# Kernel tuning notes

Hardware: AMD Instinct MI355X
Metric: run time of the kernel (lower is better)

Reference implementation:

```python
import jax, jax.numpy as jnp
import numpy as np

NUM_HEADS = 12
EPS = 1e-6


def setup_inputs() -> dict:
    key = jax.random.key(0)
    k1, k2, k3, k4 = jax.random.split(key, 4)
    N, B, D = 1025, 8, 768
    x = jax.random.normal(k1, (N, B, D), dtype=jnp.float32)
    # torch nn.Linear weights: [out_features, in_features]
    w_qkv = jax.random.normal(k2, (3 * D, D), dtype=jnp.float32) * (D ** -0.5)
    w_proj = jax.random.normal(k3, (D, D), dtype=jnp.float32) * (D ** -0.5)
    b_proj = jax.random.normal(k4, (D,), dtype=jnp.float32) * 0.01
    return {"x": x, "w_qkv": w_qkv, "w_proj": w_proj, "b_proj": b_proj}


def reference(x, w_qkv, w_proj, b_proj):
    N, B, D = x.shape
    H = NUM_HEADS
    hd = D // H
    scale = hd ** -0.5
    scale_vv = scale * 1.0  # scale_multiplier = 1.0

    xb = jnp.transpose(x, (1, 0, 2))  # [B, N, D]
    qkv = xb @ w_qkv.T  # [B, N, 3D]
    qkv = qkv.reshape(B, N, 3, H, hd).transpose(2, 0, 3, 1, 4)  # [3, B, H, N, hd]
    q, k, v = qkv[0], qkv[1], qkv[2]

    # QK path: only row 0 of out_ori survives the masking, compute just that row
    scores0 = jnp.einsum('bhqd,bhkd->bhqk', q[:, :, :1], k) * scale  # [B,H,1,N]
    attn0 = jax.nn.softmax(scores0, axis=-1)
    out0 = jnp.einsum('bhqk,bhkd->bhqd', attn0, v)  # [B,H,1,hd]

    # VV cosine path: only rows 1: survive
    vn = v / jnp.maximum(jnp.linalg.norm(v, axis=-1, keepdims=True), EPS)
    scores_vv = jnp.einsum('bhqd,bhkd->bhqk', vn[:, :, 1:], vn) * scale_vv  # [B,H,N-1,N]
    attn_vv = jax.nn.softmax(scores_vv, axis=-1)
    out_vv = jnp.einsum('bhqk,bhkd->bhqd', attn_vv, v)  # [B,H,N-1,hd]

    out = jnp.concatenate([out0, out_vv], axis=2)  # [B,H,N,hd]
    out = out.transpose(0, 2, 1, 3).reshape(B, N, D)
    out = out @ w_proj.T + b_proj
    return jnp.transpose(out, (1, 0, 2))  # [N, B, D]
```

## Files before the change

### kernel.cpp

```cpp
#include <hip/hip_runtime.h>

typedef unsigned short u16;
typedef unsigned int   u32;
typedef __attribute__((ext_vector_type(8))) short short8;
typedef __attribute__((ext_vector_type(4))) float f32x4;

#define AS1 __attribute__((address_space(1)))
#define AS3 __attribute__((address_space(3)))

#define NSEQ  1025
#define BB    8
#define DD    768
#define HH    12
#define MROWS 8200
#define MPAD  8320
#define KPAD  1088

__device__ __forceinline__ void gl2lds16(const void* g, void* l) {
  __builtin_amdgcn_global_load_lds((const AS1 u32*)g, (AS3 u32*)l, 16, 0, 0);
}
__device__ __forceinline__ u16 f2bf(float f) {
  u32 u = __float_as_uint(f);
  return (u16)((u + 0x7FFFu + ((u >> 16) & 1u)) >> 16);
}
__device__ __forceinline__ float bf2f(u16 u) { return __uint_as_float(((u32)u) << 16); }

__global__ __launch_bounds__(256) void prep(const float* __restrict__ x,
                                            const float* __restrict__ wqkv,
                                            const float* __restrict__ wproj,
                                            u16* __restrict__ xb,
                                            u16* __restrict__ wkv,
                                            u16* __restrict__ wpj) {
  const int XB_G  = MPAD * 192;
  const int WKV_G = 1536 * 192;
  const int WPJ_G = 768 * 192;
  int g = blockIdx.x * 256 + threadIdx.x;
  float4 v;
  u16* dst;
  size_t di;
  if (g < XB_G) {
    int m = g / 192, e4 = g - m * 192;
    if (m < MROWS) {
      int bb = m / NSEQ, ns = m - bb * NSEQ;
      v = ((const float4*)x)[(size_t)(ns * BB + bb) * 192 + e4];
    } else {
      v.x = v.y = v.z = v.w = 0.f;
    }
    dst = xb; di = (size_t)g;
  } else if (g < XB_G + WKV_G) {
    int r = g - XB_G;
    v = ((const float4*)wqkv)[(size_t)147456 + r];
    dst = wkv; di = (size_t)r;
  } else if (g < XB_G + WKV_G + WPJ_G) {
    int r = g - XB_G - WKV_G;
    v = ((const float4*)wproj)[r];
    dst = wpj; di = (size_t)r;
  } else {
    return;
  }
  uint2 o;
  o.x = (u32)f2bf(v.x) | ((u32)f2bf(v.y) << 16);
  o.y = (u32)f2bf(v.z) | ((u32)f2bf(v.w) << 16);
  ((uint2*)dst)[di] = o;
}

template <int MODE, int NT>
__global__ __launch_bounds__(256) void gemm_bt(const u16* __restrict__ A,
                                               const u16* __restrict__ W,
                                               u16* __restrict__ Cbf,
                                               float* __restrict__ Cf,
                                               const float* __restrict__ bias,
                                               int ldc) {
  __shared__ u16 sA[128 * 64];
  __shared__ u16 sW[128 * 64];
  const int id = blockIdx.x;
  const int rx = id & 7, qx = id >> 3;
  const int kq = qx / NT;
  const int m_t = rx + (kq << 3);
  if (m_t > 64) return;
  const int n_t = qx - kq * NT;
  const int m0 = m_t << 7, n0 = n_t << 7;

  const int tid = threadIdx.x;
  const int w = tid >> 6, lane = tid & 63;
  const int wm = w & 1, wn = w >> 1;
  const int lc = lane & 15, lr = lane >> 4;

  f32x4 zero4 = {0.f, 0.f, 0.f, 0.f};
  f32x4 acc[4][4];
#pragma unroll
  for (int i = 0; i < 4; ++i)
#pragma unroll
    for (int j = 0; j < 4; ++j) acc[i][j] = zero4;

  const int r0 = tid >> 3;
  const int ko = (tid & 7) << 3;
  const u16* gA = A + (size_t)(m0 + r0) * DD + ko;
  const u16* gW = W + (size_t)(n0 + r0) * DD + ko;
  char* lA = (char*)sA + tid * 16;
  char* lW = (char*)sW + tid * 16;

#pragma unroll 1
  for (int kt = 0; kt < 12; ++kt) {
    __syncthreads();
#pragma unroll
    for (int j = 0; j < 4; ++j) {
      gl2lds16(gA + (size_t)j * 32 * DD + kt * 64, lA + j * 4096);
      gl2lds16(gW + (size_t)j * 32 * DD + kt * 64, lW + j * 4096);
    }
    __syncthreads();
#pragma unroll
    for (int kk = 0; kk < 2; ++kk) {
      short8 af[4], wf[4];
#pragma unroll
      for (int mt = 0; mt < 4; ++mt)
        af[mt] = *(const short8*)((char*)sA + ((wm << 6) + (mt << 4) + lc) * 128 + (kk << 6) + (lr << 4));
#pragma unroll
      for (int nt = 0; nt < 4; ++nt)
        wf[nt] = *(const short8*)((char*)sW + ((wn << 6) + (nt << 4) + lc) * 128 + (kk << 6) + (lr << 4));
#pragma unroll
      for (int mt = 0; mt < 4; ++mt)
#pragma unroll
        for (int nt = 0; nt < 4; ++nt)
          acc[mt][nt] = __builtin_amdgcn_mfma_f32_16x16x32_bf16(af[mt], wf[nt], acc[mt][nt], 0, 0, 0);
    }
  }

  if (MODE == 0) {
#pragma unroll
    for (int mt = 0; mt < 4; ++mt)
#pragma unroll
      for (int r = 0; r < 4; ++r) {
        int m = m0 + (wm << 6) + (mt << 4) + (lr << 2) + r;
        if (m < MROWS) {
          size_t base = (size_t)m * ldc + n0 + (wn << 6) + lc;
#pragma unroll
          for (int nt = 0; nt < 4; ++nt) Cbf[base + (nt << 4)] = f2bf(acc[mt][nt][r]);
        }
      }
  } else {
    float b4[4];
#pragma unroll
    for (int nt = 0; nt < 4; ++nt) b4[nt] = bias[n0 + (wn << 6) + (nt << 4) + lc];
#pragma unroll
    for (int mt = 0; mt < 4; ++mt)
#pragma unroll
      for (int r = 0; r < 4; ++r) {
        int m = m0 + (wm << 6) + (mt << 4) + (lr << 2) + r;
        if (m < MROWS) {
          int bb = m / NSEQ;
          int ns = m - bb * NSEQ;
          float* o = Cf + (size_t)ns * (BB * DD) + bb * DD + n0 + (wn << 6) + lc;
#pragma unroll
          for (int nt = 0; nt < 4; ++nt) o[nt << 4] = acc[mt][nt][r] + b4[nt];
        }
      }
  }
}

__global__ __launch_bounds__(256) void q0_kernel(const float* __restrict__ x,
                                                 const float* __restrict__ wq,
                                                 float* __restrict__ q0) {
  __shared__ float red[256];
  int bid = blockIdx.x;
  int b = bid / HH, c = bid - b * HH;
  int tid = threadIdx.x;
  int dp = (c << 6) + (tid >> 2), part = tid & 3;
  const float4* x4 = (const float4*)(x + (size_t)b * DD + part * 192);
  const float4* w4 = (const float4*)(wq + (size_t)dp * DD + part * 192);
  float acc = 0.f;
#pragma unroll 4
  for (int e = 0; e < 48; ++e) {
    float4 a = x4[e], w = w4[e];
    acc += a.x * w.x + a.y * w.y + a.z * w.z + a.w * w.w;
  }
  red[tid] = acc;
  __syncthreads();
  if (part == 0) q0[b * DD + dp] = red[tid] + red[tid + 1] + red[tid + 2] + red[tid + 3];
}

__global__ __launch_bounds__(256) void transpose_v(const u16* __restrict__ kv,
                                                   u16* __restrict__ vT,
                                                   u16* __restrict__ vn) {
  __shared__ u16 tile[64][72];
  __shared__ float red[256];
  __shared__ float sInv[64];
  int bid = blockIdx.x;
  int kc = bid % 17;
  int t2 = bid / 17;
  int h = t2 % HH, b = t2 / HH;
  int tid = threadIdx.x;
  int kl = tid >> 2, dc = (tid & 3) << 4;
  int key = kc * 64 + kl;
  u32 vals[8];
  if (key < NSEQ) {
    const u32* g = (const u32*)(kv + ((size_t)b * NSEQ + key) * 1536 + DD + h * 64 + dc);
#pragma unroll
    for (int i = 0; i < 8; ++i) vals[i] = g[i];
  } else {
#pragma unroll
    for (int i = 0; i < 8; ++i) vals[i] = 0;
  }
  float part = 0.f;
#pragma unroll
  for (int i = 0; i < 8; ++i) {
    float a = bf2f((u16)(vals[i] & 0xFFFF));
    float c = bf2f((u16)(vals[i] >> 16));
    part += a * a + c * c;
    ((u32*)&tile[kl][dc])[i] = vals[i];
  }
  red[tid] = part;
  __syncthreads();
  if ((tid & 3) == 0) {
    float s = red[tid] + red[tid + 1] + red[tid + 2] + red[tid + 3];
    sInv[kl] = (key < NSEQ) ? 1.0f / fmaxf(sqrtf(s), 1e-6f) : 0.0f;
  }
  __syncthreads();
  float iv = sInv[kl];
  u32 ovn[8];
#pragma unroll
  for (int i = 0; i < 8; ++i) {
    float a = bf2f((u16)(vals[i] & 0xFFFF)) * iv;
    float c = bf2f((u16)(vals[i] >> 16)) * iv;
    ovn[i] = (u32)f2bf(a) | ((u32)f2bf(c) << 16);
  }
  u32* on = (u32*)(vn + ((size_t)(b * HH + h) * KPAD + key) * 64 + dc);
#pragma unroll
  for (int i = 0; i < 8; ++i) on[i] = ovn[i];
  int dl = tid >> 2, ks = (tid & 3) << 4;
  u32 ov[8];
#pragma unroll
  for (int i = 0; i < 8; ++i)
    ov[i] = (u32)tile[ks + 2 * i][dl] | ((u32)tile[ks + 2 * i + 1][dl] << 16);
  u16* o = vT + (size_t)(b * HH + h) * 64 * KPAD + (size_t)dl * KPAD + kc * 64 + ks;
#pragma unroll
  for (int i = 0; i < 8; ++i) ((u32*)o)[i] = ov[i];
}

__global__ __launch_bounds__(256) void row0_attn(const float* __restrict__ q0,
                                                 const u16* __restrict__ kv,
                                                 u16* __restrict__ attn) {
  __shared__ float sq[64];
  __shared__ float sc[NSEQ];
  __shared__ float red[256];
  __shared__ float rpv[32][68];
  int bid = blockIdx.x;
  int b = bid / HH, h = bid - b * HH;
  int tid = threadIdx.x;
  if (tid < 64) sq[tid] = q0[b * DD + h * 64 + tid];
  __syncthreads();
  float mx = -1e30f;
  for (int n = tid; n < NSEQ; n += 256) {
    const u32* kr = (const u32*)(kv + ((size_t)b * NSEQ + n) * 1536 + h * 64);
    float s = 0.f;
#pragma unroll
    for (int i = 0; i < 32; ++i) {
      u32 u = kr[i];
      s += bf2f((u16)(u & 0xFFFF)) * sq[2 * i] + bf2f((u16)(u >> 16)) * sq[2 * i + 1];
    }
    s *= 0.125f;
    sc[n] = s;
    mx = fmaxf(mx, s);
  }
  red[tid] = mx;
  __syncthreads();
  for (int st = 128; st > 0; st >>= 1) {
    if (tid < st) red[tid] = fmaxf(red[tid], red[tid + st]);
    __syncthreads();
  }
  mx = red[0];
  __syncthreads();
  float ds = 0.f;
  for (int n = tid; n < NSEQ; n += 256) {
    float p = __expf(sc[n] - mx);
    sc[n] = p;
    ds += p;
  }
  red[tid] = ds;
  __syncthreads();
  for (int st = 128; st > 0; st >>= 1) {
    if (tid < st) red[tid] += red[tid + st];
    __syncthreads();
  }
  float den = red[0];
  __syncthreads();

  int kp = tid >> 3, dc = (tid & 7) << 3;
  const u16* vb = kv + (size_t)b * NSEQ * 1536 + DD + h * 64 + dc;
  float acc[8];
#pragma unroll
  for (int i = 0; i < 8; ++i) acc[i] = 0.f;
#pragma unroll 4
  for (int j = 0; j < 32; ++j) {
    int n = kp + (j << 5);
    uint4 v = *(const uint4*)(vb + (size_t)n * 1536);
    float p = sc[n];
    acc[0] += p * bf2f((u16)(v.x & 0xFFFF));
    acc[1] += p * bf2f((u16)(v.x >> 16));
    acc[2] += p * bf2f((u16)(v.y & 0xFFFF));
    acc[3] += p * bf2f((u16)(v.y >> 16));
    acc[4] += p * bf2f((u16)(v.z & 0xFFFF));
    acc[5] += p * bf2f((u16)(v.z >> 16));
    acc[6] += p * bf2f((u16)(v.w & 0xFFFF));
    acc[7] += p * bf2f((u16)(v.w >> 16));
  }
  if (kp == 0) {
    uint4 v = *(const uint4*)(vb + (size_t)1024 * 1536);
    float p = sc[1024];
    acc[0] += p * bf2f((u16)(v.x & 0xFFFF));
    acc[1] += p * bf2f((u16)(v.x >> 16));
    acc[2] += p * bf2f((u16)(v.y & 0xFFFF));
    acc[3] += p * bf2f((u16)(v.y >> 16));
    acc[4] += p * bf2f((u16)(v.z & 0xFFFF));
    acc[5] += p * bf2f((u16)(v.z >> 16));
    acc[6] += p * bf2f((u16)(v.w & 0xFFFF));
    acc[7] += p * bf2f((u16)(v.w >> 16));
  }
#pragma unroll
  for (int i = 0; i < 8; ++i) rpv[kp][dc + i] = acc[i];
  __syncthreads();
  if (tid < 64) {
    float s = 0.f;
#pragma unroll
    for (int p = 0; p < 32; ++p) s += rpv[p][tid];
    attn[(size_t)b * NSEQ * DD + h * 64 + tid] = f2bf(s / den);
  }
}

__global__ __launch_bounds__(256) void vv_attn(const u16* __restrict__ vn,
                                               const u16* __restrict__ vT,
                                               u16* __restrict__ attn) {
  __shared__ u16 sQ[2 * 128 * 32];
  __shared__ u16 sK[2 * 64 * 32];
  __shared__ u16 sV[2 * 64 * 32];
  __shared__ u16 sP[128 * 72];

  const int tid = threadIdx.x, w = tid >> 6, lane = tid & 63;
  const int lc = lane & 15, lr = lane >> 4;
  const int bh = blockIdx.x;
  const int m0 = blockIdx.y << 7;
  const int b = bh / HH, h = bh - b * HH;
  const char* nb = (const char*)(vn + (size_t)bh * KPAD * 64);
  const char* tb = (const char*)(vT + (size_t)bh * 64 * KPAD);

#pragma unroll
  for (int j = 0; j < 4; ++j) {
    int lin = (w << 12) + (j << 10) + (lane << 4);
    int hf = lin >> 13, r = (lin >> 6) & 127, off = lin & 63;
    gl2lds16(nb + (size_t)(1 + m0 + r) * 128 + hf * 64 + off, (char*)sQ + lin);
  }

  f32x4 zero4 = {0.f, 0.f, 0.f, 0.f};
  f32x4 oacc[2][4];
  f32x4 dacc[2];
#pragma unroll
  for (int i = 0; i < 2; ++i) {
    dacc[i] = zero4;
#pragma unroll
    for (int j = 0; j < 4; ++j) oacc[i][j] = zero4;
  }
  short8 ones;
#pragma unroll
  for (int i = 0; i < 8; ++i) ones[i] = (short)0x3F80;

  const float CEXP = 0.1803368801111204f;

#pragma unroll 1
  for (int kt = 0; kt < 17; ++kt) {
    __syncthreads();
#pragma unroll
    for (int j = 0; j < 2; ++j) {
      int lin = (w << 11) + (j << 10) + (lane << 4);
      int hf = lin >> 12, r = (lin >> 6) & 63, off = lin & 63;
      gl2lds16(nb + (size_t)(kt * 64 + r) * 128 + hf * 64 + off, (char*)sK + lin);
      gl2lds16(tb + (size_t)r * (KPAD * 2) + kt * 128 + hf * 64 + off, (char*)sV + lin);
    }
    __syncthreads();

    f32x4 sacc[4][2];
#pragma unroll
    for (int mt = 0; mt < 4; ++mt)
#pragma unroll
      for (int nt = 0; nt < 2; ++nt) sacc[mt][nt] = zero4;
#pragma unroll
    for (int kk = 0; kk < 2; ++kk) {
      short8 ak[4], bq[2];
#pragma unroll
      for (int mt = 0; mt < 4; ++mt)
        ak[mt] = *(const short8*)((char*)sK + (kk << 12) + ((mt << 4) + lc) * 64 + (lr << 4));
#pragma unroll
      for (int nt = 0; nt < 2; ++nt)
        bq[nt] = *(const short8*)((char*)sQ + (kk << 13) + ((w << 5) + (nt << 4) + lc) * 64 + (lr << 4));
#pragma unroll
      for (int mt = 0; mt < 4; ++mt)
#pragma unroll
        for (int nt = 0; nt < 2; ++nt)
          sacc[mt][nt] = __builtin_amdgcn_mfma_f32_16x16x32_bf16(ak[mt], bq[nt], sacc[mt][nt], 0, 0, 0);
    }

#pragma unroll
    for (int mt = 0; mt < 4; ++mt) {
      int kl0 = (mt << 4) + (lr << 2);
#pragma unroll
      for (int nt = 0; nt < 2; ++nt) {
        int q = (w << 5) + (nt << 4) + lc;
        u32 a0 = __float_as_uint(__builtin_amdgcn_exp2f(sacc[mt][nt][0] * CEXP)) + 0x8000u;
        u32 a1 = __float_as_uint(__builtin_amdgcn_exp2f(sacc[mt][nt][1] * CEXP)) + 0x8000u;
        u32 a2 = __float_as_uint(__builtin_amdgcn_exp2f(sacc[mt][nt][2] * CEXP)) + 0x8000u;
        u32 a3 = __float_as_uint(__builtin_amdgcn_exp2f(sacc[mt][nt][3] * CEXP)) + 0x8000u;
        uint2 pv;
        pv.x = __builtin_amdgcn_perm(a1, a0, 0x07060302u);
        pv.y = __builtin_amdgcn_perm(a3, a2, 0x07060302u);
        if (kt == 16) {
          pv.x = (kl0 == 0) ? (pv.x & 0xFFFFu) : 0u;
          pv.y = 0u;
        }
        *(uint2*)((char*)sP + q * 144 + (kl0 << 1)) = pv;
      }
    }

#pragma unroll
    for (int kk = 0; kk < 2; ++kk) {
      short8 ap[2], bv[4];
#pragma unroll
      for (int mt = 0; mt < 2; ++mt)
        ap[mt] = *(const short8*)((char*)sP + ((w << 5) + (mt << 4) + lc) * 144 + (kk << 6) + (lr << 4));
#pragma unroll
      for (int nt = 0; nt < 4; ++nt)
        bv[nt] = *(const short8*)((char*)sV + (kk << 12) + ((nt << 4) + lc) * 64 + (lr << 4));
#pragma unroll
      for (int mt = 0; mt < 2; ++mt) {
#pragma unroll
        for (int nt = 0; nt < 4; ++nt)
          oacc[mt][nt] = __builtin_amdgcn_mfma_f32_16x16x32_bf16(ap[mt], bv[nt], oacc[mt][nt], 0, 0, 0);
        dacc[mt] = __builtin_amdgcn_mfma_f32_16x16x32_bf16(ap[mt], ones, dacc[mt], 0, 0, 0);
      }
    }
  }

#pragma unroll
  for (int mt = 0; mt < 2; ++mt) {
#pragma unroll
    for (int r = 0; r < 4; ++r) {
      int q = (w << 5) + (mt << 4) + (lr << 2) + r;
      int nseq = 1 + m0 + q;
      float rdn = 1.0f / dacc[mt][r];
      size_t obase = ((size_t)b * NSEQ + nseq) * DD + h * 64 + lc;
#pragma unroll
      for (int nt = 0; nt < 4; ++nt) attn[obase + (nt << 4)] = f2bf(oacc[mt][nt][r] * rdn);
    }
  }
}

extern "C" void kernel_launch(void* const* d_in, const int* in_sizes, int n_in,
                              void* d_out, int out_size, void* d_ws, size_t ws_size,
                              hipStream_t stream) {
  const float* x      = (const float*)d_in[0];
  const float* w_qkv  = (const float*)d_in[1];
  const float* w_proj = (const float*)d_in[2];
  const float* b_proj = (const float*)d_in[3];
  float* out = (float*)d_out;
  char* ws = (char*)d_ws;

  u16*   xb   = (u16*)(ws + 0);
  u16*   vT   = (u16*)(ws + 0);
  u16*   wkv  = (u16*)(ws + 13369344);
  u16*   wpj  = (u16*)(ws + 15728640);
  u16*   kvb  = (u16*)(ws + 16908288);
  float* q0   = (float*)(ws + 42467328);
  u16*   attn = (u16*)(ws + 42491904);
  u16*   vn   = (u16*)(ws + 55271424);

  prep<<<7968, 256, 0, stream>>>(x, w_qkv, w_proj, xb, wkv, wpj);
  gemm_bt<0, 12><<<864, 256, 0, stream>>>(xb, wkv, kvb, nullptr, nullptr, 1536);
  q0_kernel<<<96, 256, 0, stream>>>(x, w_qkv, q0);
  transpose_v<<<1632, 256, 0, stream>>>(kvb, vT, vn);
  row0_attn<<<96, 256, 0, stream>>>(q0, kvb, attn);
  vv_attn<<<dim3(96, 8), 256, 0, stream>>>(vn, vT, attn);
  gemm_bt<1, 6><<<432, 256, 0, stream>>>(attn, wpj, nullptr, out, b_proj, 768);
}
```

Before: 221.8 us.

## Fold q0 and row-0 attention into other kernels; polynomial exp in VV softmax

The separate q0 projection kernel becomes extra blocks appended to the prep kernel. The row-0 softmax attention kernel becomes an extra blockIdx.y slice of the VV attention launch, sharing one aliased shared-memory buffer. Together this removes two kernel launches and lets that small work overlap with the larger kernels. The exp2 in the VV softmax is replaced by a second-order Taylor polynomial of exp(0.125*c). This is accurate to bf16 precision because the cosine scores are bounded in [-1,1], and it drops transcendental instructions from the inner loop.

```diff
diff --git a/kernel.cpp b/kernel.cpp
--- a/kernel.cpp
+++ b/kernel.cpp
@@ -30,11 +30,31 @@
                                             const float* __restrict__ wproj,
                                             u16* __restrict__ xb,
                                             u16* __restrict__ wkv,
-                                            u16* __restrict__ wpj) {
+                                            u16* __restrict__ wpj,
+                                            float* __restrict__ q0) {
+  __shared__ float red[256];
   const int XB_G  = MPAD * 192;
   const int WKV_G = 1536 * 192;
   const int WPJ_G = 768 * 192;
-  int g = blockIdx.x * 256 + threadIdx.x;
+  int tid = threadIdx.x;
+  if (blockIdx.x >= 7968) {
+    int bid = blockIdx.x - 7968;
+    int b = bid / HH, c = bid - b * HH;
+    int dp = (c << 6) + (tid >> 2), part = tid & 3;
+    const float4* x4 = (const float4*)(x + (size_t)b * DD + part * 192);
+    const float4* w4 = (const float4*)(wqkv + (size_t)dp * DD + part * 192);
+    float acc = 0.f;
+#pragma unroll 4
+    for (int e = 0; e < 48; ++e) {
+      float4 a = x4[e], w = w4[e];
+      acc += a.x * w.x + a.y * w.y + a.z * w.z + a.w * w.w;
+    }
+    red[tid] = acc;
+    __syncthreads();
+    if (part == 0) q0[b * DD + dp] = red[tid] + red[tid + 1] + red[tid + 2] + red[tid + 3];
+    return;
+  }
+  int g = blockIdx.x * 256 + tid;
   float4 v;
   u16* dst;
   size_t di;
@@ -51,12 +71,10 @@
     int r = g - XB_G;
     v = ((const float4*)wqkv)[(size_t)147456 + r];
     dst = wkv; di = (size_t)r;
-  } else if (g < XB_G + WKV_G + WPJ_G) {
+  } else {
     int r = g - XB_G - WKV_G;
     v = ((const float4*)wproj)[r];
     dst = wpj; di = (size_t)r;
-  } else {
-    return;
   }
   uint2 o;
   o.x = (u32)f2bf(v.x) | ((u32)f2bf(v.y) << 16);
@@ -158,27 +176,6 @@
   }
 }
 
-__global__ __launch_bounds__(256) void q0_kernel(const float* __restrict__ x,
-                                                 const float* __restrict__ wq,
-                                                 float* __restrict__ q0) {
-  __shared__ float red[256];
-  int bid = blockIdx.x;
-  int b = bid / HH, c = bid - b * HH;
-  int tid = threadIdx.x;
-  int dp = (c << 6) + (tid >> 2), part = tid & 3;
-  const float4* x4 = (const float4*)(x + (size_t)b * DD + part * 192);
-  const float4* w4 = (const float4*)(wq + (size_t)dp * DD + part * 192);
-  float acc = 0.f;
-#pragma unroll 4
-  for (int e = 0; e < 48; ++e) {
-    float4 a = x4[e], w = w4[e];
-    acc += a.x * w.x + a.y * w.y + a.z * w.z + a.w * w.w;
-  }
-  red[tid] = acc;
-  __syncthreads();
-  if (part == 0) q0[b * DD + dp] = red[tid] + red[tid + 1] + red[tid + 2] + red[tid + 3];
-}
-
 __global__ __launch_bounds__(256) void transpose_v(const u16* __restrict__ kv,
                                                    u16* __restrict__ vT,
                                                    u16* __restrict__ vn) {
@@ -237,109 +234,109 @@
   for (int i = 0; i < 8; ++i) ((u32*)o)[i] = ov[i];
 }
 
-__global__ __launch_bounds__(256) void row0_attn(const float* __restrict__ q0,
-                                                 const u16* __restrict__ kv,
-                                                 u16* __restrict__ attn) {
-  __shared__ float sq[64];
-  __shared__ float sc[NSEQ];
-  __shared__ float red[256];
-  __shared__ float rpv[32][68];
-  int bid = blockIdx.x;
-  int b = bid / HH, h = bid - b * HH;
-  int tid = threadIdx.x;
-  if (tid < 64) sq[tid] = q0[b * DD + h * 64 + tid];
-  __syncthreads();
-  float mx = -1e30f;
-  for (int n = tid; n < NSEQ; n += 256) {
-    const u32* kr = (const u32*)(kv + ((size_t)b * NSEQ + n) * 1536 + h * 64);
-    float s = 0.f;
-#pragma unroll
-    for (int i = 0; i < 32; ++i) {
-      u32 u = kr[i];
-      s += bf2f((u16)(u & 0xFFFF)) * sq[2 * i] + bf2f((u16)(u >> 16)) * sq[2 * i + 1];
-    }
-    s *= 0.125f;
-    sc[n] = s;
-    mx = fmaxf(mx, s);
-  }
-  red[tid] = mx;
-  __syncthreads();
-  for (int st = 128; st > 0; st >>= 1) {
-    if (tid < st) red[tid] = fmaxf(red[tid], red[tid + st]);
-    __syncthreads();
-  }
-  mx = red[0];
-  __syncthreads();
-  float ds = 0.f;
-  for (int n = tid; n < NSEQ; n += 256) {
-    float p = __expf(sc[n] - mx);
-    sc[n] = p;
-    ds += p;
-  }
-  red[tid] = ds;
-  __syncthreads();
-  for (int st = 128; st > 0; st >>= 1) {
-    if (tid < st) red[tid] += red[tid + st];
-    __syncthreads();
-  }
-  float den = red[0];
-  __syncthreads();
-
-  int kp = tid >> 3, dc = (tid & 7) << 3;
-  const u16* vb = kv + (size_t)b * NSEQ * 1536 + DD + h * 64 + dc;
-  float acc[8];
-#pragma unroll
-  for (int i = 0; i < 8; ++i) acc[i] = 0.f;
-#pragma unroll 4
-  for (int j = 0; j < 32; ++j) {
-    int n = kp + (j << 5);
-    uint4 v = *(const uint4*)(vb + (size_t)n * 1536);
-    float p = sc[n];
-    acc[0] += p * bf2f((u16)(v.x & 0xFFFF));
-    acc[1] += p * bf2f((u16)(v.x >> 16));
-    acc[2] += p * bf2f((u16)(v.y & 0xFFFF));
-    acc[3] += p * bf2f((u16)(v.y >> 16));
-    acc[4] += p * bf2f((u16)(v.z & 0xFFFF));
-    acc[5] += p * bf2f((u16)(v.z >> 16));
-    acc[6] += p * bf2f((u16)(v.w & 0xFFFF));
-    acc[7] += p * bf2f((u16)(v.w >> 16));
-  }
-  if (kp == 0) {
-    uint4 v = *(const uint4*)(vb + (size_t)1024 * 1536);
-    float p = sc[1024];
-    acc[0] += p * bf2f((u16)(v.x & 0xFFFF));
-    acc[1] += p * bf2f((u16)(v.x >> 16));
-    acc[2] += p * bf2f((u16)(v.y & 0xFFFF));
-    acc[3] += p * bf2f((u16)(v.y >> 16));
-    acc[4] += p * bf2f((u16)(v.z & 0xFFFF));
-    acc[5] += p * bf2f((u16)(v.z >> 16));
-    acc[6] += p * bf2f((u16)(v.w & 0xFFFF));
-    acc[7] += p * bf2f((u16)(v.w >> 16));
-  }
-#pragma unroll
-  for (int i = 0; i < 8; ++i) rpv[kp][dc + i] = acc[i];
-  __syncthreads();
-  if (tid < 64) {
-    float s = 0.f;
-#pragma unroll
-    for (int p = 0; p < 32; ++p) s += rpv[p][tid];
-    attn[(size_t)b * NSEQ * DD + h * 64 + tid] = f2bf(s / den);
-  }
-}
-
 __global__ __launch_bounds__(256) void vv_attn(const u16* __restrict__ vn,
                                                const u16* __restrict__ vT,
-                                               u16* __restrict__ attn) {
-  __shared__ u16 sQ[2 * 128 * 32];
-  __shared__ u16 sK[2 * 64 * 32];
-  __shared__ u16 sV[2 * 64 * 32];
-  __shared__ u16 sP[128 * 72];
-
-  const int tid = threadIdx.x, w = tid >> 6, lane = tid & 63;
+                                               u16* __restrict__ attn,
+                                               const float* __restrict__ q0,
+                                               const u16* __restrict__ kv) {
+  __shared__ __align__(16) char smem[51200];
+  const int tid = threadIdx.x;
+  const int bh = blockIdx.x;
+  const int b = bh / HH, h = bh - b * HH;
+
+  if (blockIdx.y == 8) {
+    float* sq  = (float*)smem;
+    float* sc  = (float*)(smem + 256);
+    float* red = (float*)(smem + 4608);
+    float (*rpv)[68] = (float(*)[68])(smem + 5632);
+    if (tid < 64) sq[tid] = q0[b * DD + h * 64 + tid];
+    __syncthreads();
+    float mx = -1e30f;
+    for (int n = tid; n < NSEQ; n += 256) {
+      const u32* kr = (const u32*)(kv + ((size_t)b * NSEQ + n) * 1536 + h * 64);
+      float s = 0.f;
+#pragma unroll
+      for (int i = 0; i < 32; ++i) {
+        u32 u = kr[i];
+        s += bf2f((u16)(u & 0xFFFF)) * sq[2 * i] + bf2f((u16)(u >> 16)) * sq[2 * i + 1];
+      }
+      s *= 0.125f;
+      sc[n] = s;
+      mx = fmaxf(mx, s);
+    }
+    red[tid] = mx;
+    __syncthreads();
+    for (int st = 128; st > 0; st >>= 1) {
+      if (tid < st) red[tid] = fmaxf(red[tid], red[tid + st]);
+      __syncthreads();
+    }
+    mx = red[0];
+    __syncthreads();
+    float ds = 0.f;
+    for (int n = tid; n < NSEQ; n += 256) {
+      float p = __expf(sc[n] - mx);
+      sc[n] = p;
+      ds += p;
+    }
+    red[tid] = ds;
+    __syncthreads();
+    for (int st = 128; st > 0; st >>= 1) {
+      if (tid < st) red[tid] += red[tid + st];
+      __syncthreads();
+    }
+    float den = red[0];
+    __syncthreads();
+    int kp = tid >> 3, dc = (tid & 7) << 3;
+    const u16* vb = kv + (size_t)b * NSEQ * 1536 + DD + h * 64 + dc;
+    float acc[8];
+#pragma unroll
+    for (int i = 0; i < 8; ++i) acc[i] = 0.f;
+#pragma unroll 4
+    for (int j = 0; j < 32; ++j) {
+      int n = kp + (j << 5);
+      uint4 v = *(const uint4*)(vb + (size_t)n * 1536);
+      float p = sc[n];
+      acc[0] += p * bf2f((u16)(v.x & 0xFFFF));
+      acc[1] += p * bf2f((u16)(v.x >> 16));
+      acc[2] += p * bf2f((u16)(v.y & 0xFFFF));
+      acc[3] += p * bf2f((u16)(v.y >> 16));
+      acc[4] += p * bf2f((u16)(v.z & 0xFFFF));
+      acc[5] += p * bf2f((u16)(v.z >> 16));
+      acc[6] += p * bf2f((u16)(v.w & 0xFFFF));
+      acc[7] += p * bf2f((u16)(v.w >> 16));
+    }
+    if (kp == 0) {
+      uint4 v = *(const uint4*)(vb + (size_t)1024 * 1536);
+      float p = sc[1024];
+      acc[0] += p * bf2f((u16)(v.x & 0xFFFF));
+      acc[1] += p * bf2f((u16)(v.x >> 16));
+      acc[2] += p * bf2f((u16)(v.y & 0xFFFF));
+      acc[3] += p * bf2f((u16)(v.y >> 16));
+      acc[4] += p * bf2f((u16)(v.z & 0xFFFF));
+      acc[5] += p * bf2f((u16)(v.z >> 16));
+      acc[6] += p * bf2f((u16)(v.w & 0xFFFF));
+      acc[7] += p * bf2f((u16)(v.w >> 16));
+    }
+#pragma unroll
+    for (int i = 0; i < 8; ++i) rpv[kp][dc + i] = acc[i];
+    __syncthreads();
+    if (tid < 64) {
+      float s = 0.f;
+#pragma unroll
+      for (int p = 0; p < 32; ++p) s += rpv[p][tid];
+      attn[(size_t)b * NSEQ * DD + h * 64 + tid] = f2bf(s / den);
+    }
+    return;
+  }
+
+  char* cQ = smem;
+  char* cK = smem + 16384;
+  char* cV = smem + 24576;
+  char* cP = smem + 32768;
+
+  const int w = tid >> 6, lane = tid & 63;
   const int lc = lane & 15, lr = lane >> 4;
-  const int bh = blockIdx.x;
   const int m0 = blockIdx.y << 7;
-  const int b = bh / HH, h = bh - b * HH;
   const char* nb = (const char*)(vn + (size_t)bh * KPAD * 64);
   const char* tb = (const char*)(vT + (size_t)bh * 64 * KPAD);
 
@@ -347,7 +344,7 @@
   for (int j = 0; j < 4; ++j) {
     int lin = (w << 12) + (j << 10) + (lane << 4);
     int hf = lin >> 13, r = (lin >> 6) & 127, off = lin & 63;
-    gl2lds16(nb + (size_t)(1 + m0 + r) * 128 + hf * 64 + off, (char*)sQ + lin);
+    gl2lds16(nb + (size_t)(1 + m0 + r) * 128 + hf * 64 + off, cQ + lin);
   }
 
   f32x4 zero4 = {0.f, 0.f, 0.f, 0.f};
@@ -363,8 +360,6 @@
 #pragma unroll
   for (int i = 0; i < 8; ++i) ones[i] = (short)0x3F80;
 
-  const float CEXP = 0.1803368801111204f;
-
 #pragma unroll 1
   for (int kt = 0; kt < 17; ++kt) {
     __syncthreads();
@@ -372,8 +367,8 @@
     for (int j = 0; j < 2; ++j) {
       int lin = (w << 11) + (j << 10) + (lane << 4);
       int hf = lin >> 12, r = (lin >> 6) & 63, off = lin & 63;
-      gl2lds16(nb + (size_t)(kt * 64 + r) * 128 + hf * 64 + off, (char*)sK + lin);
-      gl2lds16(tb + (size_t)r * (KPAD * 2) + kt * 128 + hf * 64 + off, (char*)sV + lin);
+      gl2lds16(nb + (size_t)(kt * 64 + r) * 128 + hf * 64 + off, cK + lin);
+      gl2lds16(tb + (size_t)r * (KPAD * 2) + kt * 128 + hf * 64 + off, cV + lin);
     }
     __syncthreads();
 
@@ -387,10 +382,10 @@
       short8 ak[4], bq[2];
 #pragma unroll
       for (int mt = 0; mt < 4; ++mt)
-        ak[mt] = *(const short8*)((char*)sK + (kk << 12) + ((mt << 4) + lc) * 64 + (lr << 4));
+        ak[mt] = *(const short8*)(cK + (kk << 12) + ((mt << 4) + lc) * 64 + (lr << 4));
 #pragma unroll
       for (int nt = 0; nt < 2; ++nt)
-        bq[nt] = *(const short8*)((char*)sQ + (kk << 13) + ((w << 5) + (nt << 4) + lc) * 64 + (lr << 4));
+        bq[nt] = *(const short8*)(cQ + (kk << 13) + ((w << 5) + (nt << 4) + lc) * 64 + (lr << 4));
 #pragma unroll
       for (int mt = 0; mt < 4; ++mt)
 #pragma unroll
@@ -404,18 +399,20 @@
 #pragma unroll
       for (int nt = 0; nt < 2; ++nt) {
         int q = (w << 5) + (nt << 4) + lc;
-        u32 a0 = __float_as_uint(__builtin_amdgcn_exp2f(sacc[mt][nt][0] * CEXP)) + 0x8000u;
-        u32 a1 = __float_as_uint(__builtin_amdgcn_exp2f(sacc[mt][nt][1] * CEXP)) + 0x8000u;
-        u32 a2 = __float_as_uint(__builtin_amdgcn_exp2f(sacc[mt][nt][2] * CEXP)) + 0x8000u;
-        u32 a3 = __float_as_uint(__builtin_amdgcn_exp2f(sacc[mt][nt][3] * CEXP)) + 0x8000u;
+        float c0 = sacc[mt][nt][0], c1 = sacc[mt][nt][1];
+        float c2 = sacc[mt][nt][2], c3 = sacc[mt][nt][3];
+        float p0 = __builtin_fmaf(c0, __builtin_fmaf(c0, 0.0078125f, 0.125f), 1.0f);
+        float p1 = __builtin_fmaf(c1, __builtin_fmaf(c1, 0.0078125f, 0.125f), 1.0f);
+        float p2 = __builtin_fmaf(c2, __builtin_fmaf(c2, 0.0078125f, 0.125f), 1.0f);
+        float p3 = __builtin_fmaf(c3, __builtin_fmaf(c3, 0.0078125f, 0.125f), 1.0f);
         uint2 pv;
-        pv.x = __builtin_amdgcn_perm(a1, a0, 0x07060302u);
-        pv.y = __builtin_amdgcn_perm(a3, a2, 0x07060302u);
+        pv.x = __builtin_amdgcn_perm(__float_as_uint(p1), __float_as_uint(p0), 0x07060302u);
+        pv.y = __builtin_amdgcn_perm(__float_as_uint(p3), __float_as_uint(p2), 0x07060302u);
         if (kt == 16) {
           pv.x = (kl0 == 0) ? (pv.x & 0xFFFFu) : 0u;
           pv.y = 0u;
         }
-        *(uint2*)((char*)sP + q * 144 + (kl0 << 1)) = pv;
+        *(uint2*)(cP + q * 144 + (kl0 << 1)) = pv;
       }
     }
 
@@ -424,10 +421,10 @@
       short8 ap[2], bv[4];
 #pragma unroll
       for (int mt = 0; mt < 2; ++mt)
-        ap[mt] = *(const short8*)((char*)sP + ((w << 5) + (mt << 4) + lc) * 144 + (kk << 6) + (lr << 4));
+        ap[mt] = *(const short8*)(cP + ((w << 5) + (mt << 4) + lc) * 144 + (kk << 6) + (lr << 4));
 #pragma unroll
       for (int nt = 0; nt < 4; ++nt)
-        bv[nt] = *(const short8*)((char*)sV + (kk << 12) + ((nt << 4) + lc) * 64 + (lr << 4));
+        bv[nt] = *(const short8*)(cV + (kk << 12) + ((nt << 4) + lc) * 64 + (lr << 4));
 #pragma unroll
       for (int mt = 0; mt < 2; ++mt) {
 #pragma unroll
@@ -471,11 +468,9 @@
   u16*   attn = (u16*)(ws + 42491904);
   u16*   vn   = (u16*)(ws + 55271424);
 
-  prep<<<7968, 256, 0, stream>>>(x, w_qkv, w_proj, xb, wkv, wpj);
+  prep<<<8064, 256, 0, stream>>>(x, w_qkv, w_proj, xb, wkv, wpj, q0);
   gemm_bt<0, 12><<<864, 256, 0, stream>>>(xb, wkv, kvb, nullptr, nullptr, 1536);
-  q0_kernel<<<96, 256, 0, stream>>>(x, w_qkv, q0);
   transpose_v<<<1632, 256, 0, stream>>>(kvb, vT, vn);
-  row0_attn<<<96, 256, 0, stream>>>(q0, kvb, attn);
-  vv_attn<<<dim3(96, 8), 256, 0, stream>>>(vn, vT, attn);
+  vv_attn<<<dim3(96, 9), 256, 0, stream>>>(vn, vT, attn, q0, kvb);
   gemm_bt<1, 6><<<432, 256, 0, stream>>>(attn, wpj, nullptr, out, b_proj, 768);
 }
```

New measurement: 236.1 us. 6.4% more time.
